# Kernel tuning notes

Measured on AMD Instinct MI355X. Metric: run time of the kernel, lower is better.

## Reference

```python
import jax, jax.numpy as jnp
import numpy as np

B, S, D, H = 2, 2048, 2048, 16
HD = D // H          # head_dim = 128
FF = 8192            # intermediate_size
LN_EPS = 1e-05
BIT_EPS = 1e-05


def _rope_tables(seq_len, head_dim):
    inv_freq = 1.0 / (10000.0 ** (np.arange(0, head_dim, 2, dtype=np.float64) / head_dim))
    ang = np.arange(seq_len, dtype=np.float64)[:, None] * inv_freq[None, :]  # [S, HD/2]
    ang = np.concatenate([ang, ang], axis=-1)  # [S, HD]
    return jnp.asarray(np.cos(ang), jnp.float32), jnp.asarray(np.sin(ang), jnp.float32)


def setup_inputs() -> dict:
    key = jax.random.key(0)
    ks = jax.random.split(key, 9)
    hidden_states = jax.random.normal(ks[0], (B, S, D), jnp.float32)
    # causal additive mask [1, S, S]
    causal = jnp.tril(jnp.ones((S, S), bool))
    attention_mask = jnp.where(causal, 0.0, -1e9)[None].astype(jnp.float32)
    cos, sin = _rope_tables(S, HD)
    w = lambda k, o, i: jax.random.normal(k, (o, i), jnp.float32) * 0.02
    return {
        'hidden_states': hidden_states,
        'attention_mask': attention_mask,
        'cos': cos, 'sin': sin,
        'wq': w(ks[1], D, D), 'wk': w(ks[2], D, D),
        'wv': w(ks[3], D, D), 'wo': w(ks[4], D, D),
        'wg': w(ks[5], FF, D), 'wu': w(ks[6], FF, D), 'wd': w(ks[7], D, FF),
        'ln1_w': jnp.ones((D,), jnp.float32),
        'ln2_w': jnp.ones((D,), jnp.float32),
    }


def bitlinear(x, w):
    # ternarize: clamp(round(w / (mean|w| + eps)), -1, 1); int8 cast in torch
    # breaks grad through the ternary values -> stop_gradient here.
    scale = jnp.mean(jnp.abs(w))
    tern = jax.lax.stop_gradient(jnp.clip(jnp.round(w / (scale + BIT_EPS)), -1.0, 1.0))
    # dequant = ternary * mean|w|, then standard linear (x @ W^T)
    return jnp.einsum('bsi,oi->bso', x, tern * scale)


def rmsnorm(x, w, eps=LN_EPS):
    var = jnp.mean(jnp.square(x.astype(jnp.float32)), axis=-1, keepdims=True)
    return w * (x * jax.lax.rsqrt(var + eps))


def rotate_half(x):
    x1, x2 = jnp.split(x, 2, axis=-1)
    return jnp.concatenate([-x2, x1], axis=-1)


def apply_rope(q, k, cos, sin):
    # q, k: [B, S, D] -> per-head rope -> back to [B, S, D]
    qh = q.reshape(B, S, H, HD)
    kh = k.reshape(B, S, H, HD)
    c = cos[None, :, None, :]
    s = sin[None, :, None, :]
    qe = qh * c + rotate_half(qh) * s
    ke = kh * c + rotate_half(kh) * s
    return qe.reshape(B, S, D), ke.reshape(B, S, D)


def reference(hidden_states, attention_mask, cos, sin,
              wq, wk, wv, wo, wg, wu, wd, ln1_w, ln2_w):
    residual = hidden_states
    # --- attention block ---
    x = rmsnorm(hidden_states, ln1_w)
    q = bitlinear(x, wq)
    k = bitlinear(x, wk)
    v = bitlinear(x, wv)
    q, k = apply_rope(q, k, cos, sin)
    # NOTE: scores over FULL hidden dim (no head split), scaled by sqrt(head_dim),
    # exactly as in the original module.
    scores = jnp.einsum('bsd,btd->bst', q, k) / jnp.sqrt(jnp.float32(HD))
    scores = scores + attention_mask
    probs = jax.nn.softmax(scores, axis=-1)
    attn_out = jnp.einsum('bst,btd->bsd', probs, v)
    attn_out = bitlinear(attn_out, wo)
    h = residual + attn_out
    # --- MLP block ---
    residual = h
    y = rmsnorm(h, ln2_w)
    gated = bitlinear(y, wg) * bitlinear(y, wu)
    out = bitlinear(gated, wd)
    return residual + out
```

## Files before the change

### kernel.cpp

```cpp
#include <hip/hip_runtime.h>
#include <stdint.h>

#define DEV __device__ __forceinline__

typedef __attribute__((ext_vector_type(8))) short short8;
typedef __attribute__((ext_vector_type(8))) __bf16 bf16x8;
typedef __attribute__((ext_vector_type(4))) float f32x4;

DEV unsigned short f2bf(float f) {
  union { float f; unsigned int u; } v; v.f = f;
  unsigned int r = v.u + 0x7fffu + ((v.u >> 16) & 1u);
  return (unsigned short)(r >> 16);
}
DEV float bf2f(unsigned short h) {
  union { unsigned int u; float f; } v; v.u = ((unsigned int)h) << 16;
  return v.f;
}
DEV f32x4 mfma16(short8 a, short8 b, f32x4 c) {
  return __builtin_amdgcn_mfma_f32_16x16x32_bf16(
      __builtin_bit_cast(bf16x8, a), __builtin_bit_cast(bf16x8, b), c, 0, 0, 0);
}
DEV void gload_lds16(const void* g, void* lds) {
  __builtin_amdgcn_global_load_lds(
      (const __attribute__((address_space(1))) void*)g,
      (__attribute__((address_space(3))) void*)lds, 16, 0, 0);
}

struct MArgs {
  const float* src[7];
  unsigned short* dst[7];
  int n[7];
  int sidx[7];
};

__global__ __launch_bounds__(256) void absmean_partial_multi(
    MArgs a, float* __restrict__ partial) {
  const int m = blockIdx.y;
  const float4* w4 = (const float4*)a.src[m];
  const int n4 = a.n[m] >> 2;
  float s = 0.f;
  for (int i = blockIdx.x * 256 + threadIdx.x; i < n4; i += 1024 * 256) {
    float4 v = w4[i];
    s += fabsf(v.x) + fabsf(v.y) + fabsf(v.z) + fabsf(v.w);
  }
#pragma unroll
  for (int mm = 1; mm < 64; mm <<= 1) s += __shfl_xor(s, mm);
  __shared__ float red[4];
  if ((threadIdx.x & 63) == 0) red[threadIdx.x >> 6] = s;
  __syncthreads();
  if (threadIdx.x == 0)
    partial[m * 1024 + blockIdx.x] = red[0] + red[1] + red[2] + red[3];
}

__global__ __launch_bounds__(256) void absmean_final(
    const float* __restrict__ partial, float* __restrict__ scales) {
  __shared__ double red[256];
  const int m = blockIdx.x;
  double s = 0.0;
  for (int i = threadIdx.x; i < 1024; i += 256) s += (double)partial[m * 1024 + i];
  red[threadIdx.x] = s;
  __syncthreads();
  for (int t = 128; t > 0; t >>= 1) {
    if (threadIdx.x < t) red[threadIdx.x] += red[threadIdx.x + t];
    __syncthreads();
  }
  if (threadIdx.x == 0) {
    const long long cnt = (m < 4) ? 4194304ll : 16777216ll;
    scales[m] = (float)(red[0] / (double)cnt);
  }
}

__global__ __launch_bounds__(256) void quantize_multi(
    MArgs a, const float* __restrict__ scales) {
  const int m = blockIdx.y;
  const float sc = scales[a.sidx[m]];
  const float inv = 1.f / (sc + 1e-5f);
  const float4* src = (const float4*)a.src[m];
  ushort4* dst = (ushort4*)a.dst[m];
  const int n4 = a.n[m] >> 2;
  for (int i = blockIdx.x * 256 + threadIdx.x; i < n4; i += 2048 * 256) {
    float4 v = src[i];
    ushort4 o;
    o.x = f2bf(fminf(fmaxf(rintf(v.x * inv), -1.f), 1.f) * sc);
    o.y = f2bf(fminf(fmaxf(rintf(v.y * inv), -1.f), 1.f) * sc);
    o.z = f2bf(fminf(fmaxf(rintf(v.z * inv), -1.f), 1.f) * sc);
    o.w = f2bf(fminf(fmaxf(rintf(v.w * inv), -1.f), 1.f) * sc);
    dst[i] = o;
  }
}

__global__ __launch_bounds__(256) void rmsnorm_k(
    const float* __restrict__ x, const float* __restrict__ wt,
    unsigned short* __restrict__ out) {
  const long long t = blockIdx.x;
  const float* xr = x + t * 2048;
  const int i0 = threadIdx.x * 8;
  float4 a = *(const float4*)(xr + i0);
  float4 b = *(const float4*)(xr + i0 + 4);
  float ss = a.x * a.x + a.y * a.y + a.z * a.z + a.w * a.w +
             b.x * b.x + b.y * b.y + b.z * b.z + b.w * b.w;
#pragma unroll
  for (int m = 1; m < 64; m <<= 1) ss += __shfl_xor(ss, m);
  __shared__ float red[4];
  if ((threadIdx.x & 63) == 0) red[threadIdx.x >> 6] = ss;
  __syncthreads();
  float tot = red[0] + red[1] + red[2] + red[3];
  float rs = rsqrtf(tot * (1.f / 2048.f) + 1e-5f);
  float4 wa = *(const float4*)(wt + i0);
  float4 wb = *(const float4*)(wt + i0 + 4);
  ushort4 o1, o2;
  o1.x = f2bf(a.x * wa.x * rs); o1.y = f2bf(a.y * wa.y * rs);
  o1.z = f2bf(a.z * wa.z * rs); o1.w = f2bf(a.w * wa.w * rs);
  o2.x = f2bf(b.x * wb.x * rs); o2.y = f2bf(b.y * wb.y * rs);
  o2.z = f2bf(b.z * wb.z * rs); o2.w = f2bf(b.w * wb.w * rs);
  *(ushort4*)(out + t * 2048 + i0) = o1;
  *(ushort4*)(out + t * 2048 + i0 + 4) = o2;
}

__global__ __launch_bounds__(256) void rope_k(
    const unsigned short* __restrict__ qkv, const float* __restrict__ cosT,
    const float* __restrict__ sinT, unsigned short* __restrict__ qr,
    unsigned short* __restrict__ kr, unsigned short* __restrict__ vt) {
  const long long gid = (long long)blockIdx.x * 256 + threadIdx.x;
  const int t = (int)(gid >> 10);
  const int r = (int)(gid & 1023);
  const int h = r >> 6, d = r & 63;
  const int s = t & 2047, b = t >> 11;
  const unsigned short* row = qkv + (long long)t * 6144;
  const float c = cosT[s * 128 + d], sn = sinT[s * 128 + d];
  const int col = h * 128 + d;
  const float SC = 0.08838834764831845f;
  float q1 = bf2f(row[col]), q2 = bf2f(row[col + 64]);
  float k1 = bf2f(row[2048 + col]), k2 = bf2f(row[2048 + col + 64]);
  long long ob = (long long)t * 2048 + col;
  qr[ob] = f2bf((q1 * c - q2 * sn) * SC);
  qr[ob + 64] = f2bf((q2 * c + q1 * sn) * SC);
  kr[ob] = f2bf(k1 * c - k2 * sn);
  kr[ob + 64] = f2bf(k2 * c + k1 * sn);
  vt[((long long)b * 2048 + col) * 2048 + s] = row[4096 + col];
  vt[((long long)b * 2048 + col + 64) * 2048 + s] = row[4096 + col + 64];
}

__global__ __launch_bounds__(256) void softmax_causal(
    const float* __restrict__ scores, unsigned short* __restrict__ probs) {
  const int r = blockIdx.x;
  const int s = r & 2047;
  const float* src = scores + (long long)r * 2048;
  unsigned short* dst = probs + (long long)r * 2048;
  const int L = s + 1;
  __shared__ float red[4];
  float mx = -1e30f;
  for (int j = threadIdx.x; j < L; j += 256) mx = fmaxf(mx, src[j]);
#pragma unroll
  for (int m = 1; m < 64; m <<= 1) mx = fmaxf(mx, __shfl_xor(mx, m));
  if ((threadIdx.x & 63) == 0) red[threadIdx.x >> 6] = mx;
  __syncthreads();
  mx = fmaxf(fmaxf(red[0], red[1]), fmaxf(red[2], red[3]));
  float sum = 0.f;
  for (int j = threadIdx.x; j < L; j += 256) sum += __expf(src[j] - mx);
  __syncthreads();
#pragma unroll
  for (int m = 1; m < 64; m <<= 1) sum += __shfl_xor(sum, m);
  if ((threadIdx.x & 63) == 0) red[threadIdx.x >> 6] = sum;
  __syncthreads();
  const float inv = 1.f / (red[0] + red[1] + red[2] + red[3]);
  for (int j = threadIdx.x; j < 2048; j += 256)
    dst[j] = (j < L) ? f2bf(__expf(src[j] - mx) * inv) : (unsigned short)0;
}

template <int EPI, int CAUSAL>
__global__ __launch_bounds__(256) void gemm_nt(
    const unsigned short* __restrict__ A, const unsigned short* __restrict__ Bw,
    void* __restrict__ Cp, int M, int N, int K,
    long long sAz, long long sBz, long long sCz) {
  const long long m0 = (long long)blockIdx.y * 128;
  const long long n0 = (long long)blockIdx.x * 128;
  if (CAUSAL == 1 && n0 > m0 + 127) return;
  __shared__ __align__(16) unsigned short sA[2][128 * 32];
  __shared__ __align__(16) unsigned short sB[2][128 * 32];
  const int tid = threadIdx.x;
  const int w = tid >> 6, l = tid & 63;
  const long long z = blockIdx.z;
  A += z * sAz;
  Bw += z * sBz;
  const long long cofs = z * sCz;
  const int wr = w >> 1, wc = w & 1;
  const int lrow = l & 15, lk = (l >> 4) * 8;

  f32x4 acc[4][4] = {};
  int nk = K >> 5;
  if (CAUSAL == 2) nk = (int)((m0 + 128) >> 5);
  int cur = 0;

  auto stage = [&](int buf, int k0) {
#pragma unroll
    for (int i = 0; i < 2; ++i) {
      const int flat = (w * 2 + i) * 64 + l;
      const int row = flat >> 2;
      const int col = (flat & 3) * 8;
      gload_lds16(&A[(m0 + row) * K + k0 + col], (char*)&sA[buf][0] + (w * 2 + i) * 1024);
      gload_lds16(&Bw[(n0 + row) * K + k0 + col], (char*)&sB[buf][0] + (w * 2 + i) * 1024);
    }
  };

  stage(0, 0);
  __syncthreads();
  for (int kt = 0; kt < nk; ++kt) {
    if (kt + 1 < nk) stage(cur ^ 1, (kt + 1) << 5);
    short8 af[4], bfr[4];
#pragma unroll
    for (int m = 0; m < 4; ++m)
      af[m] = *(const short8*)&sA[cur][(wr * 64 + m * 16 + lrow) * 32 + lk];
#pragma unroll
    for (int n = 0; n < 4; ++n)
      bfr[n] = *(const short8*)&sB[cur][(wc * 64 + n * 16 + lrow) * 32 + lk];
#pragma unroll
    for (int m = 0; m < 4; ++m)
#pragma unroll
      for (int n = 0; n < 4; ++n)
        acc[m][n] = mfma16(af[m], bfr[n], acc[m][n]);
    __syncthreads();
    cur ^= 1;
  }

  const int orow = (l >> 4) * 4, ocol = l & 15;
#pragma unroll
  for (int m = 0; m < 4; ++m)
#pragma unroll
    for (int n = 0; n < 4; ++n)
#pragma unroll
      for (int r = 0; r < 4; ++r) {
        long long gr = m0 + wr * 64 + m * 16 + orow + r;
        long long gc = n0 + wc * 64 + n * 16 + ocol;
        long long idx = cofs + gr * N + gc;
        float v = acc[m][n][r];
        if (EPI == 0) ((unsigned short*)Cp)[idx] = f2bf(v);
        else ((float*)Cp)[idx] = v;
      }
}

template <int EPI>
__global__ __launch_bounds__(512, 2) void gemm256(
    const unsigned short* __restrict__ A, const unsigned short* __restrict__ Bw,
    void* __restrict__ Cp, const void* __restrict__ Ep,
    int N, int K, int nbx, int kLen, int nChunks, long long zCout) {
  __shared__ __align__(16) unsigned short lds[4 * 2 * 8192];
  __shared__ __align__(16) unsigned short ldsDummy[512];
  const int tid = threadIdx.x;
  const int wid = tid >> 6, l = tid & 63;
  const int wr = wid >> 2, wcn = wid & 3;

  const int nwg = gridDim.x;
  const int q8 = nwg >> 3;
  const int lin = (blockIdx.x & 7) * q8 + (blockIdx.x >> 3);
  const int t32 = lin >> 5, r32 = lin & 31;
  const int tpr = nbx >> 3;
  const int tm = t32 / tpr, tn = t32 - tm * tpr;
  const long long m0 = (long long)(tm * 4 + (r32 >> 3)) * 256;
  const long long n0 = (long long)(tn * 8 + (r32 & 7)) * 256;
  const int z = blockIdx.z;
  const long long kbase = (long long)z * kLen;
  const long long zofs = (long long)z * zCout;

  const int stRow = (l >> 2);
  const int stCol = (((l & 3) ^ ((l >> 3) & 3))) * 8;
  auto stage = [&](int chunk, int mat) {
    char* base = (char*)lds + (((chunk & 3) * 2 + mat) * 16384);
    const unsigned short* src = mat ? Bw : A;
    const long long rb = mat ? n0 : m0;
    if (chunk < nChunks) {
      const long long kcol = kbase + (long long)chunk * 32 + stCol;
#pragma unroll
      for (int i = 0; i < 2; ++i) {
        const int row = (wid * 2 + i) * 16 + stRow;
        gload_lds16(&src[(rb + row) * K + kcol], base + (wid * 2 + i) * 1024);
      }
    } else {
#pragma unroll
      for (int i = 0; i < 2; ++i) gload_lds16(&src[rb * K], (char*)ldsDummy);
    }
  };

  const int ar = l & 15;
  const int rj = ((l >> 4) ^ ((l >> 1) & 3)) << 4;

  f32x4 acc[8][4] = {};

  stage(0, 0); stage(0, 1);
  stage(1, 0); stage(1, 1);
  stage(2, 0); stage(2, 1);
  asm volatile("s_waitcnt vmcnt(8)" ::: "memory");
  __builtin_amdgcn_s_barrier();

  for (int c = 0; c < nChunks; ++c) {
    const int slot = c & 3;
    const char* sA = (const char*)lds + (slot * 2 + 0) * 16384;
    const char* sB = (const char*)lds + (slot * 2 + 1) * 16384;
    short8 af[4], bf[4];
#pragma unroll
    for (int m = 0; m < 4; ++m)
      af[m] = *(const short8*)(sA + (wr * 128 + m * 16 + ar) * 64 + rj);
#pragma unroll
    for (int n = 0; n < 4; ++n)
      bf[n] = *(const short8*)(sB + (wcn * 64 + n * 16 + ar) * 64 + rj);
    stage(c + 3, 0);
    __builtin_amdgcn_s_barrier();
    asm volatile("s_waitcnt lgkmcnt(0)" ::: "memory");
    __builtin_amdgcn_sched_barrier(0);
    __builtin_amdgcn_s_setprio(1);
#pragma unroll
    for (int m = 0; m < 4; ++m)
#pragma unroll
      for (int n = 0; n < 4; ++n) acc[m][n] = mfma16(af[m], bf[n], acc[m][n]);
    __builtin_amdgcn_s_setprio(0);
    __builtin_amdgcn_s_barrier();
#pragma unroll
    for (int m = 0; m < 4; ++m)
      af[m] = *(const short8*)(sA + (wr * 128 + (m + 4) * 16 + ar) * 64 + rj);
    stage(c + 3, 1);
    __builtin_amdgcn_s_barrier();
    asm volatile("s_waitcnt lgkmcnt(0)" ::: "memory");
    __builtin_amdgcn_sched_barrier(0);
    __builtin_amdgcn_s_setprio(1);
#pragma unroll
    for (int m = 0; m < 4; ++m)
#pragma unroll
      for (int n = 0; n < 4; ++n)
        acc[m + 4][n] = mfma16(af[m], bf[n], acc[m + 4][n]);
    __builtin_amdgcn_s_setprio(0);
    asm volatile("s_waitcnt vmcnt(8)" ::: "memory");
    __builtin_amdgcn_s_barrier();
  }
  asm volatile("s_waitcnt vmcnt(0)" ::: "memory");
  __builtin_amdgcn_s_barrier();

  const int orow = (l >> 4) * 4, ocol = l & 15;
#pragma unroll
  for (int m = 0; m < 8; ++m)
#pragma unroll
    for (int n = 0; n < 4; ++n)
#pragma unroll
      for (int r = 0; r < 4; ++r) {
        const long long gr = m0 + wr * 128 + m * 16 + orow + r;
        const long long gc = n0 + wcn * 64 + n * 16 + ocol;
        const long long idx = zofs + gr * N + gc;
        const float v = acc[m][n][r];
        if (EPI == 0) {
          ((unsigned short*)Cp)[idx] = f2bf(v);
        } else if (EPI == 2) {
          ((unsigned short*)Cp)[idx] = f2bf(bf2f(((const unsigned short*)Ep)[idx]) * v);
        } else {
          ((float*)Cp)[idx] = v;
        }
      }
}

__global__ __launch_bounds__(256) void combine2(
    const float* __restrict__ ep, const float* __restrict__ p,
    float* __restrict__ out, long long n4) {
  const float4* e4 = (const float4*)ep;
  const float4* p4 = (const float4*)p;
  float4* o4 = (float4*)out;
  for (long long i = blockIdx.x * 256 + threadIdx.x; i < n4; i += 2048 * 256) {
    float4 a = e4[i], b = p4[i], c = p4[i + n4];
    float4 o;
    o.x = a.x + b.x + c.x; o.y = a.y + b.y + c.y;
    o.z = a.z + b.z + c.z; o.w = a.w + b.w + c.w;
    o4[i] = o;
  }
}

extern "C" void kernel_launch(void* const* d_in, const int* in_sizes, int n_in,
                              void* d_out, int out_size, void* d_ws, size_t ws_size,
                              hipStream_t stream) {
  (void)in_sizes; (void)n_in; (void)out_size; (void)ws_size;
  const float* hidden = (const float*)d_in[0];
  const float* cosT = (const float*)d_in[2];
  const float* sinT = (const float*)d_in[3];
  const float* wq = (const float*)d_in[4];
  const float* wk = (const float*)d_in[5];
  const float* wv = (const float*)d_in[6];
  const float* wo = (const float*)d_in[7];
  const float* wg = (const float*)d_in[8];
  const float* wu = (const float*)d_in[9];
  const float* wd = (const float*)d_in[10];
  const float* ln1 = (const float*)d_in[11];
  const float* ln2 = (const float*)d_in[12];

  const size_t MB = 1ull << 20;
  char* ws = (char*)d_ws;
  unsigned short* xn    = (unsigned short*)(ws + 0);
  unsigned short* wqkvq = (unsigned short*)(ws + 16 * MB);
  unsigned short* qkv   = (unsigned short*)(ws + 40 * MB);
  unsigned short* qrb   = (unsigned short*)(ws + 88 * MB);
  unsigned short* krb   = (unsigned short*)(ws + 104 * MB);
  unsigned short* vtb   = (unsigned short*)(ws + 120 * MB);
  float*          scoresB = (float*)(ws + 0);
  unsigned short* probsB  = (unsigned short*)(ws + 40 * MB);
  float*          part   = (float*)(ws + 0);
  unsigned short* wgq   = (unsigned short*)(ws + 0);
  unsigned short* wuq   = (unsigned short*)(ws + 32 * MB);
  unsigned short* gbuf  = (unsigned short*)(ws + 64 * MB);
  unsigned short* attnb = (unsigned short*)(ws + 136 * MB);
  unsigned short* woq   = (unsigned short*)(ws + 152 * MB);
  float*          hbuf  = (float*)(ws + 160 * MB);
  unsigned short* ybuf  = (unsigned short*)(ws + 192 * MB);
  unsigned short* gated = (unsigned short*)(ws + 208 * MB);
  unsigned short* wdq   = (unsigned short*)(ws + 272 * MB);
  float* wspart         = (float*)(ws + 304 * MB);
  float* scales         = (float*)(ws + 304 * MB + 32768);

  MArgs am;
  am.src[0] = wq; am.src[1] = wk; am.src[2] = wv; am.src[3] = wo;
  am.src[4] = wg; am.src[5] = wu; am.src[6] = wd;
  am.n[0] = am.n[1] = am.n[2] = am.n[3] = 4194304;
  am.n[4] = am.n[5] = am.n[6] = 16777216;
  for (int i = 0; i < 7; ++i) { am.dst[i] = nullptr; am.sidx[i] = i; }
  absmean_partial_multi<<<dim3(1024, 7), 256, 0, stream>>>(am, wspart);
  absmean_final<<<7, 256, 0, stream>>>(wspart, scales);

  MArgs qe;
  qe.src[0] = wq; qe.dst[0] = wqkvq;            qe.n[0] = 4194304;  qe.sidx[0] = 0;
  qe.src[1] = wk; qe.dst[1] = wqkvq + 4194304;  qe.n[1] = 4194304;  qe.sidx[1] = 1;
  qe.src[2] = wv; qe.dst[2] = wqkvq + 8388608;  qe.n[2] = 4194304;  qe.sidx[2] = 2;
  qe.src[3] = wo; qe.dst[3] = woq;              qe.n[3] = 4194304;  qe.sidx[3] = 3;
  qe.src[4] = wd; qe.dst[4] = wdq;              qe.n[4] = 16777216; qe.sidx[4] = 6;
  qe.src[5] = wq; qe.dst[5] = nullptr; qe.n[5] = 0; qe.sidx[5] = 0;
  qe.src[6] = wq; qe.dst[6] = nullptr; qe.n[6] = 0; qe.sidx[6] = 0;
  quantize_multi<<<dim3(2048, 5), 256, 0, stream>>>(qe, scales);

  rmsnorm_k<<<4096, 256, 0, stream>>>(hidden, ln1, xn);

  gemm256<0><<<dim3(384, 1, 1), 512, 0, stream>>>(
      xn, wqkvq, qkv, nullptr, 6144, 2048, 24, 2048, 64, 0);

  rope_k<<<16384, 256, 0, stream>>>(qkv, cosT, sinT, qrb, krb, vtb);

  gemm_nt<4, 1><<<dim3(16, 16, 2), 256, 0, stream>>>(
      qrb, krb, scoresB, 2048, 2048, 2048, 4194304, 4194304, 4194304);
  softmax_causal<<<4096, 256, 0, stream>>>(scoresB, probsB);
  gemm_nt<0, 2><<<dim3(16, 16, 2), 256, 0, stream>>>(
      probsB, vtb, attnb, 2048, 2048, 2048, 4194304, 4194304, 4194304);

  gemm256<4><<<dim3(128, 1, 2), 512, 0, stream>>>(
      attnb, woq, part, nullptr, 2048, 2048, 8, 1024, 32, 8388608);
  combine2<<<2048, 256, 0, stream>>>(hidden, part, hbuf, 2097152);

  MArgs ql;
  ql.src[0] = wg; ql.dst[0] = wgq; ql.n[0] = 16777216; ql.sidx[0] = 4;
  ql.src[1] = wu; ql.dst[1] = wuq; ql.n[1] = 16777216; ql.sidx[1] = 5;
  for (int i = 2; i < 7; ++i) { ql.src[i] = wg; ql.dst[i] = nullptr; ql.n[i] = 0; ql.sidx[i] = 0; }
  quantize_multi<<<dim3(2048, 2), 256, 0, stream>>>(ql, scales);

  rmsnorm_k<<<4096, 256, 0, stream>>>(hbuf, ln2, ybuf);

  gemm256<0><<<dim3(512, 1, 1), 512, 0, stream>>>(
      ybuf, wgq, gbuf, nullptr, 8192, 2048, 32, 2048, 64, 0);
  gemm256<2><<<dim3(512, 1, 1), 512, 0, stream>>>(
      ybuf, wuq, gated, gbuf, 8192, 2048, 32, 2048, 64, 0);

  gemm256<4><<<dim3(128, 1, 2), 512, 0, stream>>>(
      gated, wdq, part, nullptr, 2048, 8192, 8, 4096, 128, 8388608);
  combine2<<<2048, 256, 0, stream>>>(hbuf, part, (float*)d_out, 2097152);
}
```

Before: 880.0 us.

## Switch GEMMs to 32x32 MFMA, reuse 256-tile kernel for attention, vectorize softmax

The 256x256 tiled GEMM now issues 32x32x16 bf16 MFMAs instead of 16x16x32, with new swizzled LDS fragment indexing and epilogue mapping. The small 128-tile gemm_nt kernel for QK^T and PV is removed. Those products now run on the 256-tile kernel, which gains per-z strides and causal tile skipping and K-truncation. Softmax is rewritten to load each row once into registers with vector loads and write vectorized bf16 output, avoiding re-reading the scores. The risks are coarser causal granularity, which wastes more work on diagonal tiles, and fewer workgroups for the attention GEMMs.

Result: slower. 949.3 us (+7.9%).

```diff
diff --git a/kernel.cpp b/kernel.cpp
--- a/kernel.cpp
+++ b/kernel.cpp
@@ -5,7 +5,7 @@
 
 typedef __attribute__((ext_vector_type(8))) short short8;
 typedef __attribute__((ext_vector_type(8))) __bf16 bf16x8;
-typedef __attribute__((ext_vector_type(4))) float f32x4;
+typedef __attribute__((ext_vector_type(16))) float f32x16;
 
 DEV unsigned short f2bf(float f) {
   union { float f; unsigned int u; } v; v.f = f;
@@ -16,8 +16,8 @@
   union { unsigned int u; float f; } v; v.u = ((unsigned int)h) << 16;
   return v.f;
 }
-DEV f32x4 mfma16(short8 a, short8 b, f32x4 c) {
-  return __builtin_amdgcn_mfma_f32_16x16x32_bf16(
+DEV f32x16 mfma32(short8 a, short8 b, f32x16 c) {
+  return __builtin_amdgcn_mfma_f32_32x32x16_bf16(
       __builtin_bit_cast(bf16x8, a), __builtin_bit_cast(bf16x8, b), c, 0, 0, 0);
 }
 DEV void gload_lds16(const void* g, void* lds) {
@@ -148,102 +148,48 @@
   const float* src = scores + (long long)r * 2048;
   unsigned short* dst = probs + (long long)r * 2048;
   const int L = s + 1;
-  __shared__ float red[4];
+  const int j0 = threadIdx.x * 8;
+  float4 a = *(const float4*)(src + j0);
+  float4 b = *(const float4*)(src + j0 + 4);
+  float v[8] = {a.x, a.y, a.z, a.w, b.x, b.y, b.z, b.w};
   float mx = -1e30f;
-  for (int j = threadIdx.x; j < L; j += 256) mx = fmaxf(mx, src[j]);
+#pragma unroll
+  for (int i = 0; i < 8; ++i) {
+    if (j0 + i >= L) v[i] = -1e30f;
+    mx = fmaxf(mx, v[i]);
+  }
 #pragma unroll
   for (int m = 1; m < 64; m <<= 1) mx = fmaxf(mx, __shfl_xor(mx, m));
-  if ((threadIdx.x & 63) == 0) red[threadIdx.x >> 6] = mx;
+  __shared__ float redM[4], redS[4];
+  if ((threadIdx.x & 63) == 0) redM[threadIdx.x >> 6] = mx;
   __syncthreads();
-  mx = fmaxf(fmaxf(red[0], red[1]), fmaxf(red[2], red[3]));
+  mx = fmaxf(fmaxf(redM[0], redM[1]), fmaxf(redM[2], redM[3]));
   float sum = 0.f;
-  for (int j = threadIdx.x; j < L; j += 256) sum += __expf(src[j] - mx);
+#pragma unroll
+  for (int i = 0; i < 8; ++i) {
+    v[i] = (j0 + i < L) ? __expf(v[i] - mx) : 0.f;
+    sum += v[i];
+  }
+#pragma unroll
+  for (int m = 1; m < 64; m <<= 1) sum += __shfl_xor(sum, m);
+  if ((threadIdx.x & 63) == 0) redS[threadIdx.x >> 6] = sum;
   __syncthreads();
-#pragma unroll
-  for (int m = 1; m < 64; m <<= 1) sum += __shfl_xor(sum, m);
-  if ((threadIdx.x & 63) == 0) red[threadIdx.x >> 6] = sum;
-  __syncthreads();
-  const float inv = 1.f / (red[0] + red[1] + red[2] + red[3]);
-  for (int j = threadIdx.x; j < 2048; j += 256)
-    dst[j] = (j < L) ? f2bf(__expf(src[j] - mx) * inv) : (unsigned short)0;
+  const float inv = 1.f / (redS[0] + redS[1] + redS[2] + redS[3]);
+  ushort4 o1, o2;
+  o1.x = f2bf(v[0] * inv); o1.y = f2bf(v[1] * inv);
+  o1.z = f2bf(v[2] * inv); o1.w = f2bf(v[3] * inv);
+  o2.x = f2bf(v[4] * inv); o2.y = f2bf(v[5] * inv);
+  o2.z = f2bf(v[6] * inv); o2.w = f2bf(v[7] * inv);
+  *(ushort4*)(dst + j0) = o1;
+  *(ushort4*)(dst + j0 + 4) = o2;
 }
 
 template <int EPI, int CAUSAL>
-__global__ __launch_bounds__(256) void gemm_nt(
-    const unsigned short* __restrict__ A, const unsigned short* __restrict__ Bw,
-    void* __restrict__ Cp, int M, int N, int K,
-    long long sAz, long long sBz, long long sCz) {
-  const long long m0 = (long long)blockIdx.y * 128;
-  const long long n0 = (long long)blockIdx.x * 128;
-  if (CAUSAL == 1 && n0 > m0 + 127) return;
-  __shared__ __align__(16) unsigned short sA[2][128 * 32];
-  __shared__ __align__(16) unsigned short sB[2][128 * 32];
-  const int tid = threadIdx.x;
-  const int w = tid >> 6, l = tid & 63;
-  const long long z = blockIdx.z;
-  A += z * sAz;
-  Bw += z * sBz;
-  const long long cofs = z * sCz;
-  const int wr = w >> 1, wc = w & 1;
-  const int lrow = l & 15, lk = (l >> 4) * 8;
-
-  f32x4 acc[4][4] = {};
-  int nk = K >> 5;
-  if (CAUSAL == 2) nk = (int)((m0 + 128) >> 5);
-  int cur = 0;
-
-  auto stage = [&](int buf, int k0) {
-#pragma unroll
-    for (int i = 0; i < 2; ++i) {
-      const int flat = (w * 2 + i) * 64 + l;
-      const int row = flat >> 2;
-      const int col = (flat & 3) * 8;
-      gload_lds16(&A[(m0 + row) * K + k0 + col], (char*)&sA[buf][0] + (w * 2 + i) * 1024);
-      gload_lds16(&Bw[(n0 + row) * K + k0 + col], (char*)&sB[buf][0] + (w * 2 + i) * 1024);
-    }
-  };
-
-  stage(0, 0);
-  __syncthreads();
-  for (int kt = 0; kt < nk; ++kt) {
-    if (kt + 1 < nk) stage(cur ^ 1, (kt + 1) << 5);
-    short8 af[4], bfr[4];
-#pragma unroll
-    for (int m = 0; m < 4; ++m)
-      af[m] = *(const short8*)&sA[cur][(wr * 64 + m * 16 + lrow) * 32 + lk];
-#pragma unroll
-    for (int n = 0; n < 4; ++n)
-      bfr[n] = *(const short8*)&sB[cur][(wc * 64 + n * 16 + lrow) * 32 + lk];
-#pragma unroll
-    for (int m = 0; m < 4; ++m)
-#pragma unroll
-      for (int n = 0; n < 4; ++n)
-        acc[m][n] = mfma16(af[m], bfr[n], acc[m][n]);
-    __syncthreads();
-    cur ^= 1;
-  }
-
-  const int orow = (l >> 4) * 4, ocol = l & 15;
-#pragma unroll
-  for (int m = 0; m < 4; ++m)
-#pragma unroll
-    for (int n = 0; n < 4; ++n)
-#pragma unroll
-      for (int r = 0; r < 4; ++r) {
-        long long gr = m0 + wr * 64 + m * 16 + orow + r;
-        long long gc = n0 + wc * 64 + n * 16 + ocol;
-        long long idx = cofs + gr * N + gc;
-        float v = acc[m][n][r];
-        if (EPI == 0) ((unsigned short*)Cp)[idx] = f2bf(v);
-        else ((float*)Cp)[idx] = v;
-      }
-}
-
-template <int EPI>
 __global__ __launch_bounds__(512, 2) void gemm256(
     const unsigned short* __restrict__ A, const unsigned short* __restrict__ Bw,
     void* __restrict__ Cp, const void* __restrict__ Ep,
-    int N, int K, int nbx, int kLen, int nChunks, long long zCout) {
+    int N, int K, int nbx, int kLen, int ngTot,
+    long long sAz, long long sBz, long long zCout) {
   __shared__ __align__(16) unsigned short lds[4 * 2 * 8192];
   __shared__ __align__(16) unsigned short ldsDummy[512];
   const int tid = threadIdx.x;
@@ -258,9 +204,17 @@
   const int tm = t32 / tpr, tn = t32 - tm * tpr;
   const long long m0 = (long long)(tm * 4 + (r32 >> 3)) * 256;
   const long long n0 = (long long)(tn * 8 + (r32 & 7)) * 256;
+  if (CAUSAL == 1 && n0 > m0) return;
   const int z = blockIdx.z;
+  A += z * sAz;
+  Bw += z * sBz;
   const long long kbase = (long long)z * kLen;
   const long long zofs = (long long)z * zCout;
+  int ng = ngTot;
+  if (CAUSAL == 2) {
+    const int lim = (int)((m0 + 256) >> 5);
+    ng = lim < ng ? lim : ng;
+  }
 
   const int stRow = (l >> 2);
   const int stCol = (((l & 3) ^ ((l >> 3) & 3))) * 8;
@@ -268,7 +222,7 @@
     char* base = (char*)lds + (((chunk & 3) * 2 + mat) * 16384);
     const unsigned short* src = mat ? Bw : A;
     const long long rb = mat ? n0 : m0;
-    if (chunk < nChunks) {
+    if (chunk < ng) {
       const long long kcol = kbase + (long long)chunk * 32 + stCol;
 #pragma unroll
       for (int i = 0; i < 2; ++i) {
@@ -281,10 +235,10 @@
     }
   };
 
-  const int ar = l & 15;
-  const int rj = ((l >> 4) ^ ((l >> 1) & 3)) << 4;
-
-  f32x4 acc[8][4] = {};
+  const int rl31 = l & 31, rhi = l >> 5;
+  const int rsw = (rl31 >> 1) & 3;
+
+  f32x16 acc[4][2] = {};
 
   stage(0, 0); stage(0, 1);
   stage(1, 0); stage(1, 1);
@@ -292,41 +246,55 @@
   asm volatile("s_waitcnt vmcnt(8)" ::: "memory");
   __builtin_amdgcn_s_barrier();
 
-  for (int c = 0; c < nChunks; ++c) {
+  for (int c = 0; c < ng; ++c) {
     const int slot = c & 3;
     const char* sA = (const char*)lds + (slot * 2 + 0) * 16384;
     const char* sB = (const char*)lds + (slot * 2 + 1) * 16384;
-    short8 af[4], bf[4];
-#pragma unroll
-    for (int m = 0; m < 4; ++m)
-      af[m] = *(const short8*)(sA + (wr * 128 + m * 16 + ar) * 64 + rj);
-#pragma unroll
-    for (int n = 0; n < 4; ++n)
-      bf[n] = *(const short8*)(sB + (wcn * 64 + n * 16 + ar) * 64 + rj);
+    short8 af[2][2], bfr[2][2];
+#pragma unroll
+    for (int m = 0; m < 2; ++m)
+#pragma unroll
+      for (int s = 0; s < 2; ++s)
+        af[m][s] = *(const short8*)(sA + (wr * 128 + m * 32 + rl31) * 64 +
+                                    (((s * 2 + rhi) ^ rsw) << 4));
+#pragma unroll
+    for (int n = 0; n < 2; ++n)
+#pragma unroll
+      for (int s = 0; s < 2; ++s)
+        bfr[n][s] = *(const short8*)(sB + (wcn * 64 + n * 32 + rl31) * 64 +
+                                     (((s * 2 + rhi) ^ rsw) << 4));
     stage(c + 3, 0);
     __builtin_amdgcn_s_barrier();
     asm volatile("s_waitcnt lgkmcnt(0)" ::: "memory");
     __builtin_amdgcn_sched_barrier(0);
     __builtin_amdgcn_s_setprio(1);
 #pragma unroll
-    for (int m = 0; m < 4; ++m)
-#pragma unroll
-      for (int n = 0; n < 4; ++n) acc[m][n] = mfma16(af[m], bf[n], acc[m][n]);
+    for (int m = 0; m < 2; ++m)
+#pragma unroll
+      for (int n = 0; n < 2; ++n)
+#pragma unroll
+        for (int s = 0; s < 2; ++s)
+          acc[m][n] = mfma32(af[m][s], bfr[n][s], acc[m][n]);
     __builtin_amdgcn_s_setprio(0);
     __builtin_amdgcn_s_barrier();
 #pragma unroll
-    for (int m = 0; m < 4; ++m)
-      af[m] = *(const short8*)(sA + (wr * 128 + (m + 4) * 16 + ar) * 64 + rj);
+    for (int m = 0; m < 2; ++m)
+#pragma unroll
+      for (int s = 0; s < 2; ++s)
+        af[m][s] = *(const short8*)(sA + (wr * 128 + (m + 2) * 32 + rl31) * 64 +
+                                    (((s * 2 + rhi) ^ rsw) << 4));
     stage(c + 3, 1);
     __builtin_amdgcn_s_barrier();
     asm volatile("s_waitcnt lgkmcnt(0)" ::: "memory");
     __builtin_amdgcn_sched_barrier(0);
     __builtin_amdgcn_s_setprio(1);
 #pragma unroll
-    for (int m = 0; m < 4; ++m)
-#pragma unroll
-      for (int n = 0; n < 4; ++n)
-        acc[m + 4][n] = mfma16(af[m], bf[n], acc[m + 4][n]);
+    for (int m = 0; m < 2; ++m)
+#pragma unroll
+      for (int n = 0; n < 2; ++n)
+#pragma unroll
+        for (int s = 0; s < 2; ++s)
+          acc[m + 2][n] = mfma32(af[m][s], bfr[n][s], acc[m + 2][n]);
     __builtin_amdgcn_s_setprio(0);
     asm volatile("s_waitcnt vmcnt(8)" ::: "memory");
     __builtin_amdgcn_s_barrier();
@@ -334,15 +302,16 @@
   asm volatile("s_waitcnt vmcnt(0)" ::: "memory");
   __builtin_amdgcn_s_barrier();
 
-  const int orow = (l >> 4) * 4, ocol = l & 15;
-#pragma unroll
-  for (int m = 0; m < 8; ++m)
-#pragma unroll
-    for (int n = 0; n < 4; ++n)
-#pragma unroll
-      for (int r = 0; r < 4; ++r) {
-        const long long gr = m0 + wr * 128 + m * 16 + orow + r;
-        const long long gc = n0 + wcn * 64 + n * 16 + ocol;
+  const long long cm = m0 + wr * 128;
+  const long long cn = n0 + wcn * 64;
+#pragma unroll
+  for (int m = 0; m < 4; ++m)
+#pragma unroll
+    for (int n = 0; n < 2; ++n)
+#pragma unroll
+      for (int r = 0; r < 16; ++r) {
+        const long long gr = cm + m * 32 + (r & 3) + 8 * (r >> 2) + 4 * rhi;
+        const long long gc = cn + n * 32 + rl31;
         const long long idx = zofs + gr * N + gc;
         const float v = acc[m][n][r];
         if (EPI == 0) {
@@ -431,19 +400,19 @@
 
   rmsnorm_k<<<4096, 256, 0, stream>>>(hidden, ln1, xn);
 
-  gemm256<0><<<dim3(384, 1, 1), 512, 0, stream>>>(
-      xn, wqkvq, qkv, nullptr, 6144, 2048, 24, 2048, 64, 0);
+  gemm256<0, 0><<<dim3(384, 1, 1), 512, 0, stream>>>(
+      xn, wqkvq, qkv, nullptr, 6144, 2048, 24, 2048, 64, 0, 0, 0);
 
   rope_k<<<16384, 256, 0, stream>>>(qkv, cosT, sinT, qrb, krb, vtb);
 
-  gemm_nt<4, 1><<<dim3(16, 16, 2), 256, 0, stream>>>(
-      qrb, krb, scoresB, 2048, 2048, 2048, 4194304, 4194304, 4194304);
+  gemm256<4, 1><<<dim3(64, 1, 2), 512, 0, stream>>>(
+      qrb, krb, scoresB, nullptr, 2048, 2048, 8, 0, 64, 4194304, 4194304, 4194304);
   softmax_causal<<<4096, 256, 0, stream>>>(scoresB, probsB);
-  gemm_nt<0, 2><<<dim3(16, 16, 2), 256, 0, stream>>>(
-      probsB, vtb, attnb, 2048, 2048, 2048, 4194304, 4194304, 4194304);
-
-  gemm256<4><<<dim3(128, 1, 2), 512, 0, stream>>>(
-      attnb, woq, part, nullptr, 2048, 2048, 8, 1024, 32, 8388608);
+  gemm256<0, 2><<<dim3(64, 1, 2), 512, 0, stream>>>(
+      probsB, vtb, attnb, nullptr, 2048, 2048, 8, 0, 64, 4194304, 4194304, 4194304);
+
+  gemm256<4, 0><<<dim3(128, 1, 2), 512, 0, stream>>>(
+      attnb, woq, part, nullptr, 2048, 2048, 8, 1024, 32, 0, 0, 8388608);
   combine2<<<2048, 256, 0, stream>>>(hidden, part, hbuf, 2097152);
 
   MArgs ql;
@@ -454,12 +423,12 @@
 
   rmsnorm_k<<<4096, 256, 0, stream>>>(hbuf, ln2, ybuf);
 
-  gemm256<0><<<dim3(512, 1, 1), 512, 0, stream>>>(
-      ybuf, wgq, gbuf, nullptr, 8192, 2048, 32, 2048, 64, 0);
-  gemm256<2><<<dim3(512, 1, 1), 512, 0, stream>>>(
-      ybuf, wuq, gated, gbuf, 8192, 2048, 32, 2048, 64, 0);
-
-  gemm256<4><<<dim3(128, 1, 2), 512, 0, stream>>>(
-      gated, wdq, part, nullptr, 2048, 8192, 8, 4096, 128, 8388608);
+  gemm256<0, 0><<<dim3(512, 1, 1), 512, 0, stream>>>(
+      ybuf, wgq, gbuf, nullptr, 8192, 2048, 32, 2048, 64, 0, 0, 0);
+  gemm256<2, 0><<<dim3(512, 1, 1), 512, 0, stream>>>(
+      ybuf, wuq, gated, gbuf, 8192, 2048, 32, 2048, 64, 0, 0, 0);
+
+  gemm256<4, 0><<<dim3(128, 1, 2), 512, 0, stream>>>(
+      gated, wdq, part, nullptr, 2048, 8192, 8, 4096, 128, 0, 0, 8388608);
   combine2<<<2048, 256, 0, stream>>>(hbuf, part, (float*)d_out, 2097152);
 }
```
